# Kernel tuning notes

Hardware: AMD Instinct MI355X
Metric: run time of the kernel (lower is better)

## Reference

```python
import jax, jax.numpy as jnp
import numpy as np

D = 768        # d_model
NH = 12        # num_heads
HD = D // NH   # head_dim = 64
MH = 3072      # mlp_hidden = 4*d_model
EPS = 1e-5
SCALE = HD ** -0.5


def _ln(x, w, b):
    m = jnp.mean(x, axis=-1, keepdims=True)
    v = jnp.mean(jnp.square(x - m), axis=-1, keepdims=True)
    return (x - m) * jax.lax.rsqrt(v + EPS) * w + b


def _rotate_half(x):
    x1, x2 = jnp.split(x, 2, axis=-1)
    return jnp.concatenate([-x2, x1], axis=-1)


def _rope_cos_sin(n, dim):
    inv = 1.0 / (10000.0 ** (jnp.arange(0, dim, 2, dtype=jnp.float32) / dim))
    ang = jnp.arange(n, dtype=jnp.float32)[:, None] * inv[None, :]
    ang = jnp.concatenate([ang, ang], axis=-1)  # (n, dim)
    return jnp.cos(ang), jnp.sin(ang)


def _mlp(x, w1, b1, w2, b2):
    return jax.nn.gelu(x @ w1 + b1, approximate=False) @ w2 + b2


def _attn(q, k, v):
    # q,k,v: (B, S, NH, HD)
    a = jnp.einsum('bqhd,bkhd->bhqk', q, k) * SCALE
    a = jax.nn.softmax(a, axis=-1)
    return jnp.einsum('bhqk,bkhd->bqhd', a, v)


def _spatial_attn(x, qkv_w, proj_w, proj_b):
    # x: (B, T, H, W, C); attention over H*W per frame with 2D RoPE
    B, T, H, W, C = x.shape
    BT, S = B * T, H * W
    qkv = x.reshape(BT, S, C) @ qkv_w
    q, k, v = jnp.split(qkv, 3, axis=-1)
    q = q.reshape(BT, S, NH, HD)
    k = k.reshape(BT, S, NH, HD)
    v = v.reshape(BT, S, NH, HD)
    half = HD // 2
    cos_h, sin_h = _rope_cos_sin(H, half)
    cos_w, sin_w = _rope_cos_sin(W, half)

    def rope2d(t):
        t = t.reshape(BT, H, W, NH, HD)
        t1, t2 = t[..., :half], t[..., half:]
        ch, sh = cos_h[None, :, None, None, :], sin_h[None, :, None, None, :]
        cw, sw = cos_w[None, None, :, None, :], sin_w[None, None, :, None, :]
        t1 = t1 * ch + _rotate_half(t1) * sh  # rotate by row position
        t2 = t2 * cw + _rotate_half(t2) * sw  # rotate by col position
        return jnp.concatenate([t1, t2], axis=-1).reshape(BT, S, NH, HD)

    out = _attn(rope2d(q), rope2d(k), v).reshape(BT, S, C) @ proj_w + proj_b
    return out.reshape(B, T, H, W, C)


def _temporal_attn(vp, vf, ap, af, qkv_w, proj_w, proj_b):
    # vp/vf: (B, T, S, C); ap/af: (B, T, C); joint attention over concatenated time axis
    B, T_p, S, C = vp.shape
    T_f = vf.shape[1]
    BS = B * S
    vps = vp.transpose(0, 2, 1, 3).reshape(BS, T_p, C)
    vfs = vf.transpose(0, 2, 1, 3).reshape(BS, T_f, C)
    aps = jnp.broadcast_to(ap[:, None], (B, S, T_p, C)).reshape(BS, T_p, C)
    afs = jnp.broadcast_to(af[:, None], (B, S, T_f, C)).reshape(BS, T_f, C)
    tok = jnp.concatenate([vps, vfs, aps, afs], axis=1)
    TT = tok.shape[1]
    qkv = tok @ qkv_w
    q, k, v = jnp.split(qkv, 3, axis=-1)
    q = q.reshape(BS, TT, NH, HD)
    k = k.reshape(BS, TT, NH, HD)
    v = v.reshape(BS, TT, NH, HD)
    cos, sin = _rope_cos_sin(TT, HD)
    rope1d = lambda t: t * cos[None, :, None, :] + _rotate_half(t) * sin[None, :, None, :]
    out = _attn(rope1d(q), rope1d(k), v).reshape(BS, TT, C) @ proj_w + proj_b
    vp_o = out[:, :T_p].reshape(B, S, T_p, C).transpose(0, 2, 1, 3)
    vf_o = out[:, T_p:T_p + T_f].reshape(B, S, T_f, C).transpose(0, 2, 1, 3)
    ap_o = out[:, T_p + T_f:T_p + T_f + T_p].reshape(B, S, T_p, C).mean(axis=1)
    af_o = out[:, T_p + T_f + T_p:].reshape(B, S, T_f, C).mean(axis=1)
    return vp_o, vf_o, ap_o, af_o


def _forward(v_p, v_f, a_p, a_f,
             sa_qkv_w, sa_proj_w, sa_proj_b,
             smlp_w1, smlp_b1, smlp_w2, smlp_b2,
             ta_qkv_w, ta_proj_w, ta_proj_b,
             ln1_w, ln1_b, ln2_w, ln2_b, ln3_w, ln3_b, ln4_w, ln4_b,
             fvp_w1, fvp_b1, fvp_w2, fvp_b2,
             fvf_w1, fvf_b1, fvf_w2, fvf_b2,
             fap_w1, fap_b1, fap_w2, fap_b2,
             faf_w1, faf_b1, faf_w2, faf_b2):
    # 1) shared spatial attention (video streams) + 2) shared video MLP, pre-norm residual
    def video_stage(x):
        x = x + _spatial_attn(_ln(x, ln1_w, ln1_b), sa_qkv_w, sa_proj_w, sa_proj_b)
        x = x + _mlp(_ln(x, ln2_w, ln2_b), smlp_w1, smlp_b1, smlp_w2, smlp_b2)
        return x
    v_p = video_stage(v_p)
    v_f = video_stage(v_f)
    B, T_p, H, W, C = v_p.shape
    T_f = v_f.shape[1]
    S = H * W
    vp_s = v_p.reshape(B, T_p, S, C)
    vf_s = v_f.reshape(B, T_f, S, C)
    # 3) joint temporal attention across all streams with 1D RoPE
    dvp, dvf, dap, daf = _temporal_attn(
        _ln(vp_s, ln3_w, ln3_b), _ln(vf_s, ln3_w, ln3_b),
        _ln(a_p, ln3_w, ln3_b), _ln(a_f, ln3_w, ln3_b),
        ta_qkv_w, ta_proj_w, ta_proj_b)
    vp_s = vp_s + dvp
    vf_s = vf_s + dvf
    a_p = a_p + dap
    a_f = a_f + daf
    # 4) distinct final MLP per stream
    vp_s = vp_s + _mlp(_ln(vp_s, ln4_w, ln4_b), fvp_w1, fvp_b1, fvp_w2, fvp_b2)
    vf_s = vf_s + _mlp(_ln(vf_s, ln4_w, ln4_b), fvf_w1, fvf_b1, fvf_w2, fvf_b2)
    a_p = a_p + _mlp(_ln(a_p, ln4_w, ln4_b), fap_w1, fap_b1, fap_w2, fap_b2)
    a_f = a_f + _mlp(_ln(a_f, ln4_w, ln4_b), faf_w1, faf_b1, faf_w2, faf_b2)
    return (vp_s.reshape(B, T_p, H, W, C), vf_s.reshape(B, T_f, H, W, C), a_p, a_f)


def setup_inputs() -> dict:
    B, T, H, W = 4, 8, 16, 16
    key = jax.random.key(0)
    kit = iter(jax.random.split(key, 48))
    def nrm(shape, s=0.02):
        return jax.random.normal(next(kit), shape, jnp.float32) * s
    inp = {
        'v_p': jax.random.normal(next(kit), (B, T, H, W, D), jnp.float32),
        'v_f': jax.random.normal(next(kit), (B, T, H, W, D), jnp.float32),
        'a_p': jax.random.normal(next(kit), (B, T, D), jnp.float32),
        'a_f': jax.random.normal(next(kit), (B, T, D), jnp.float32),
        'sa_qkv_w': nrm((D, 3 * D)),
        'sa_proj_w': nrm((D, D)),
        'sa_proj_b': jnp.zeros((D,), jnp.float32),
        'smlp_w1': nrm((D, MH)), 'smlp_b1': jnp.zeros((MH,), jnp.float32),
        'smlp_w2': nrm((MH, D)), 'smlp_b2': jnp.zeros((D,), jnp.float32),
        'ta_qkv_w': nrm((D, 3 * D)),
        'ta_proj_w': nrm((D, D)),
        'ta_proj_b': jnp.zeros((D,), jnp.float32),
    }
    for nm in ('ln1', 'ln2', 'ln3', 'ln4'):
        inp[nm + '_w'] = jnp.ones((D,), jnp.float32)
        inp[nm + '_b'] = jnp.zeros((D,), jnp.float32)
    for nm in ('fvp', 'fvf', 'fap', 'faf'):
        inp[nm + '_w1'] = nrm((D, MH))
        inp[nm + '_b1'] = jnp.zeros((MH,), jnp.float32)
        inp[nm + '_w2'] = nrm((MH, D))
        inp[nm + '_b2'] = jnp.zeros((D,), jnp.float32)
    return inp


def reference(v_p, v_f, a_p, a_f,
              sa_qkv_w, sa_proj_w, sa_proj_b,
              smlp_w1, smlp_b1, smlp_w2, smlp_b2,
              ta_qkv_w, ta_proj_w, ta_proj_b,
              ln1_w, ln1_b, ln2_w, ln2_b, ln3_w, ln3_b, ln4_w, ln4_b,
              fvp_w1, fvp_b1, fvp_w2, fvp_b2,
              fvf_w1, fvf_b1, fvf_w2, fvf_b2,
              fap_w1, fap_b1, fap_w2, fap_b2,
              faf_w1, faf_b1, faf_w2, faf_b2):
    return _forward(v_p, v_f, a_p, a_f,
                    sa_qkv_w, sa_proj_w, sa_proj_b,
                    smlp_w1, smlp_b1, smlp_w2, smlp_b2,
                    ta_qkv_w, ta_proj_w, ta_proj_b,
                    ln1_w, ln1_b, ln2_w, ln2_b, ln3_w, ln3_b, ln4_w, ln4_b,
                    fvp_w1, fvp_b1, fvp_w2, fvp_b2,
                    fvf_w1, fvf_b1, fvf_w2, fvf_b2,
                    fap_w1, fap_b1, fap_w2, fap_b2,
                    faf_w1, faf_b1, faf_w2, faf_b2)
```

## Files before the change

kernel.cpp:

```cpp
#include <hip/hip_runtime.h>
#include <hip/hip_bf16.h>

#define D 768
#define NH 12
#define HD 64
#define MH 3072
#define LN_EPS 1e-5f
#define ATT_SCALE 0.125f

typedef unsigned short u16;
typedef unsigned int u32;
typedef short short8 __attribute__((ext_vector_type(8)));
typedef float f32x4 __attribute__((ext_vector_type(4)));

__device__ __forceinline__ float b2f(u16 u){
  union { u32 i; float f; } x; x.i = ((u32)u) << 16; return x.f;
}
__device__ __forceinline__ u16 f2b(float f){
  u32 x = __float_as_uint(f);
  x += 0x7fffu + ((x >> 16) & 1u);
  return (u16)(x >> 16);
}
__device__ __forceinline__ u32 packb(float a, float b){
  return (u32)f2b(a) | ((u32)f2b(b) << 16);
}
__device__ __forceinline__ bool is_f32(const u32* __restrict__ probe){
  return probe[0] == 0x3F800000u;
}

__device__ __forceinline__ void gload_lds16(const u16* g, u16* l){
  auto const* gp = reinterpret_cast<u32 const __attribute__((address_space(1)))*>(
      reinterpret_cast<uintptr_t>(g));
  auto* lp = reinterpret_cast<u32 __attribute__((address_space(3)))*>(
      reinterpret_cast<uintptr_t>(l));
  __builtin_amdgcn_global_load_lds(gp, lp, 16, 0, 0);
}

__device__ __forceinline__ void up8(uint4 u, float* f){
  f[0] = b2f((u16)(u.x & 0xffff)); f[1] = b2f((u16)(u.x >> 16));
  f[2] = b2f((u16)(u.y & 0xffff)); f[3] = b2f((u16)(u.y >> 16));
  f[4] = b2f((u16)(u.z & 0xffff)); f[5] = b2f((u16)(u.z >> 16));
  f[6] = b2f((u16)(u.w & 0xffff)); f[7] = b2f((u16)(u.w >> 16));
}

__global__ void k_in2f(const void* __restrict__ in, float* __restrict__ out, int n4,
                       const u32* __restrict__ probe){
  int i = blockIdx.x * 256 + threadIdx.x;
  if (i >= n4) return;
  if (is_f32(probe)){
    ((float4*)out)[i] = ((const float4*)in)[i];
  } else {
    uint2 u = ((const uint2*)in)[i];
    float4 f;
    f.x = b2f((u16)(u.x & 0xffff)); f.y = b2f((u16)(u.x >> 16));
    f.z = b2f((u16)(u.y & 0xffff)); f.w = b2f((u16)(u.y >> 16));
    ((float4*)out)[i] = f;
  }
}

__global__ void k_out(const float* __restrict__ in, void* __restrict__ out,
                      size_t elem_off, int n4, const u32* __restrict__ probe){
  int i = blockIdx.x * 256 + threadIdx.x;
  if (i >= n4) return;
  float4 f = ((const float4*)in)[i];
  if (is_f32(probe)){
    ((float4*)((float*)out + elem_off))[i] = f;
  } else {
    uint2 u;
    u.x = packb(f.x, f.y);
    u.y = packb(f.z, f.w);
    ((uint2*)((u16*)out + elem_off))[i] = u;
  }
}

__global__ __launch_bounds__(256) void k_transp(const void* __restrict__ W,
    u16* __restrict__ WT, int K, int N, const u32* __restrict__ probe)
{
  __shared__ u16 t[32][33];
  bool wf = is_f32(probe);
  int k0 = blockIdx.x * 32, n0 = blockIdx.y * 32;
  int tx = threadIdx.x & 31, ty = threadIdx.x >> 5;
  #pragma unroll
  for (int i = 0; i < 4; i++){
    int k = k0 + ty + i*8;
    float v = wf ? ((const float*)W)[(size_t)k*N + n0 + tx]
                 : b2f(((const u16*)W)[(size_t)k*N + n0 + tx]);
    t[ty + i*8][tx] = f2b(v);
  }
  __syncthreads();
  #pragma unroll
  for (int i = 0; i < 4; i++){
    int n = n0 + ty + i*8;
    WT[(size_t)n*K + k0 + tx] = t[tx][ty + i*8];
  }
}

__global__ __launch_bounds__(256) void k_ln(const float* __restrict__ X,
    const void* __restrict__ w, const void* __restrict__ b,
    u16* __restrict__ Y, int nrows, const u32* __restrict__ probe)
{
  bool wf = is_f32(probe);
  int wv = threadIdx.x >> 6, lane = threadIdx.x & 63;
  int row = blockIdx.x * 4 + wv;
  if (row >= nrows) return;
  const float* x = X + (size_t)row * D;
  float v[12];
  float s = 0.f;
  #pragma unroll
  for (int i = 0; i < 12; i++){ v[i] = x[lane + i*64]; s += v[i]; }
  #pragma unroll
  for (int m = 32; m; m >>= 1) s += __shfl_xor(s, m);
  float mean = s * (1.f/768.f);
  float q = 0.f;
  #pragma unroll
  for (int i = 0; i < 12; i++){ float d0 = v[i] - mean; q += d0*d0; }
  #pragma unroll
  for (int m = 32; m; m >>= 1) q += __shfl_xor(q, m);
  float rstd = rsqrtf(q * (1.f/768.f) + LN_EPS);
  u16* y = Y + (size_t)row * D;
  #pragma unroll
  for (int i = 0; i < 12; i++){
    int c = lane + i*64;
    float wc = wf ? ((const float*)w)[c] : b2f(((const u16*)w)[c]);
    float bc = wf ? ((const float*)b)[c] : b2f(((const u16*)b)[c]);
    y[c] = f2b((v[i] - mean) * rstd * wc + bc);
  }
}

#define BM 128
#define BK 64

template<int EPI, int GUARD, int BNN>
__global__ __launch_bounds__(256, 2) void k_gemm(
    const u16* __restrict__ A, const u16* __restrict__ WT,
    const void* __restrict__ bias, void* __restrict__ Cout,
    const float* __restrict__ resid, const u32* __restrict__ probe,
    int M, int N, int K)
{
  constexpr int AT = (BNN == 128) ? 4 : 2;
  __shared__ __align__(16) u16 lA[2][BM][BK];
  __shared__ __align__(16) u16 lB[2][BNN][BK];
  bool wf = is_f32(probe);
  int tid = threadIdx.x;
  int m0 = blockIdx.y * BM, n0 = blockIdx.x * BNN;
  int wv = tid >> 6, lane = tid & 63, quad = lane >> 4, r = lane & 15;
  int wm = (BNN == 128) ? (wv >> 1) * 64 : wv * 32;
  int wn = (BNN == 128) ? (wv & 1) * 64 : 0;

  f32x4 acc[AT][4] = {};

  int lrow = lane >> 3;
  int lcol = (lane & 7) * 8;
  int nt = K / BK;

  auto stage = [&](int t, int bi){
    int k0 = t * BK;
    if (GUARD){
      int a_r = tid >> 3;
      int a_c = (tid & 7) * 8;
      #pragma unroll
      for (int p = 0; p < 4; p++){
        int row = p*32 + a_r;
        uint4 val = make_uint4(0u,0u,0u,0u);
        if (m0 + row < M)
          val = *(const uint4*)(A + (size_t)(m0+row)*K + k0 + a_c);
        *(uint4*)&lA[bi][row][a_c] = val;
      }
    } else {
      #pragma unroll
      for (int p = 0; p < 4; p++){
        int c = wv*4 + p;
        gload_lds16(A + (size_t)(m0 + c*8 + lrow)*K + k0 + lcol, &lA[bi][c*8][0]);
      }
    }
    #pragma unroll
    for (int p = 0; p < BNN/32; p++){
      int c = wv*(BNN/32) + p;
      gload_lds16(WT + (size_t)(n0 + c*8 + lrow)*K + k0 + lcol, &lB[bi][c*8][0]);
    }
  };

  stage(0, 0);
  __syncthreads();

  for (int t = 0; t < nt; ++t){
    int cur = t & 1;
    if (t + 1 < nt) stage(t + 1, cur ^ 1);
    #pragma unroll
    for (int kk = 0; kk < 2; kk++){
      short8 af[AT], bf[4];
      #pragma unroll
      for (int i = 0; i < AT; i++)
        af[i] = *(const short8*)&lA[cur][wm + i*16 + r][kk*32 + quad*8];
      #pragma unroll
      for (int j = 0; j < 4; j++)
        bf[j] = *(const short8*)&lB[cur][wn + j*16 + r][kk*32 + quad*8];
      #pragma unroll
      for (int i = 0; i < AT; i++)
        #pragma unroll
        for (int j = 0; j < 4; j++)
          acc[i][j] = __builtin_amdgcn_mfma_f32_16x16x32_bf16(af[i], bf[j], acc[i][j], 0, 0, 0);
    }
    __syncthreads();
  }

  #pragma unroll
  for (int i = 0; i < AT; i++){
    #pragma unroll
    for (int reg = 0; reg < 4; reg++){
      int row = m0 + wm + i*16 + quad*4 + reg;
      if (row >= M) continue;
      #pragma unroll
      for (int j = 0; j < 4; j++){
        int col = n0 + wn + j*16 + r;
        float v = acc[i][j][reg];
        size_t idx = (size_t)row * N + col;
        if (EPI == 0){
          ((u16*)Cout)[idx] = f2b(v);
        } else if (EPI == 1){
          v += wf ? ((const float*)bias)[col] : b2f(((const u16*)bias)[col]);
          v = 0.5f * v * (1.f + erff(v * 0.70710678f));
          ((u16*)Cout)[idx] = f2b(v);
        } else {
          v += (wf ? ((const float*)bias)[col] : b2f(((const u16*)bias)[col])) + resid[idx];
          ((float*)Cout)[idx] = v;
        }
      }
    }
  }
}

__global__ __launch_bounds__(512, 2) void k_spat_attn(
    const u16* __restrict__ QKV, u16* __restrict__ OUT)
{
  __shared__ __align__(16) u16 lK[256*64];
  __shared__ __align__(16) u16 lVT[64*256];
  __shared__ __align__(16) u16 lQP[256*64];
  int bt = blockIdx.x / NH, h = blockIdx.x % NH;
  int tid = threadIdx.x;

  {
    int token = tid >> 1, half = tid & 1;
    int dbase = half * 32;
    float pos = half ? (float)(token & 15) : (float)(token >> 4);
    const u16* src = QKV + (size_t)(bt*256 + token) * 2304 + h*64 + dbase;
    float q[32], k[32];
    #pragma unroll
    for (int i = 0; i < 4; i++){
      up8(((const uint4*)src)[i],         &q[i*8]);
      up8(((const uint4*)(src + 768))[i], &k[i*8]);
    }
    #pragma unroll
    for (int j = 0; j < 16; j++){
      float inv = exp2f(-(float)j * 0.8304820237721841f);
      float sn, cs; __sincosf(pos * inv, &sn, &cs);
      { float a = q[j], b = q[j+16]; q[j] = a*cs - b*sn; q[j+16] = b*cs + a*sn; }
      { float a = k[j], b = k[j+16]; k[j] = a*cs - b*sn; k[j+16] = b*cs + a*sn; }
    }
    #pragma unroll
    for (int g = 0; g < 4; g++){
      int slot = (half*4 + g) ^ (token & 7);
      u32 wq[4], wk[4];
      #pragma unroll
      for (int p2 = 0; p2 < 4; p2++){
        wq[p2] = packb(q[g*8+p2*2] * ATT_SCALE, q[g*8+p2*2+1] * ATT_SCALE);
        wk[p2] = packb(k[g*8+p2*2], k[g*8+p2*2+1]);
      }
      *(uint4*)&lQP[token*64 + slot*8] = *(uint4*)wq;
      *(uint4*)&lK [token*64 + slot*8] = *(uint4*)wk;
    }
    uint4 vv[4];
    #pragma unroll
    for (int i = 0; i < 4; i++) vv[i] = ((const uint4*)(src + 1536))[i];
    #pragma unroll
    for (int i = 0; i < 32; i++){
      int d = dbase + i;
      u32 w = ((const u32*)vv)[i >> 1];
      lVT[d*256 + (((token>>3) ^ (d&7))*8) + (token&7)] =
          (i & 1) ? (u16)(w >> 16) : (u16)(w & 0xffff);
    }
  }
  __syncthreads();

  int wv = tid >> 6, lane = tid & 63, quad = lane >> 4, r = lane & 15;

  short8 qa[2][2];
  #pragma unroll
  for (int qt = 0; qt < 2; qt++)
    #pragma unroll
    for (int dc = 0; dc < 2; dc++){
      int q = wv*32 + qt*16 + r;
      int slot = (dc*4 + quad) ^ (q & 7);
      qa[qt][dc] = *(const short8*)&lQP[q*64 + slot*8];
    }
  __syncthreads();

  u16* Pw = &lQP[wv * 1024];
  const short8 ones = {(short)0x3F80,(short)0x3F80,(short)0x3F80,(short)0x3F80,
                       (short)0x3F80,(short)0x3F80,(short)0x3F80,(short)0x3F80};
  f32x4 acc[2][4] = {};
  f32x4 lacc[2] = {};
  float mrow[2][4];
  #pragma unroll
  for (int qt = 0; qt < 2; qt++)
    #pragma unroll
    for (int rg = 0; rg < 4; rg++) mrow[qt][rg] = -1e30f;

  for (int c = 0; c < 8; c++){
    f32x4 s[2][2] = {};
    #pragma unroll
    for (int dc = 0; dc < 2; dc++){
      short8 bk[2];
      #pragma unroll
      for (int kt = 0; kt < 2; kt++){
        int kk = c*32 + kt*16 + r;
        int slot = (dc*4 + quad) ^ (kk & 7);
        bk[kt] = *(const short8*)&lK[kk*64 + slot*8];
      }
      #pragma unroll
      for (int qt = 0; qt < 2; qt++)
        #pragma unroll
        for (int kt = 0; kt < 2; kt++)
          s[qt][kt] = __builtin_amdgcn_mfma_f32_16x16x32_bf16(qa[qt][dc], bk[kt], s[qt][kt], 0, 0, 0);
    }
    #pragma unroll
    for (int qt = 0; qt < 2; qt++){
      float corr[4];
      #pragma unroll
      for (int rg = 0; rg < 4; rg++){
        float mx = fmaxf(s[qt][0][rg], s[qt][1][rg]);
        #pragma unroll
        for (int msk = 1; msk <= 8; msk <<= 1) mx = fmaxf(mx, __shfl_xor(mx, msk));
        float mn = fmaxf(mrow[qt][rg], mx);
        corr[rg] = __expf(mrow[qt][rg] - mn);
        mrow[qt][rg] = mn;
      }
      #pragma unroll
      for (int rg = 0; rg < 4; rg++) lacc[qt][rg] *= corr[rg];
      #pragma unroll
      for (int dt = 0; dt < 4; dt++)
        #pragma unroll
        for (int rg = 0; rg < 4; rg++) acc[qt][dt][rg] *= corr[rg];
      #pragma unroll
      for (int kt = 0; kt < 2; kt++)
        #pragma unroll
        for (int rg = 0; rg < 4; rg++){
          float p = __expf(s[qt][kt][rg] - mrow[qt][rg]);
          int qq = qt*16 + quad*4 + rg;
          int kk = kt*16 + r;
          Pw[qq*32 + (((kk>>3) ^ ((qq>>1)&3))*8) + (kk&7)] = f2b(p);
        }
    }
    short8 pa[2];
    #pragma unroll
    for (int qt = 0; qt < 2; qt++){
      int qq = qt*16 + r;
      int slot = quad ^ ((qq>>1)&3);
      pa[qt] = *(const short8*)&Pw[qq*32 + slot*8];
      lacc[qt] = __builtin_amdgcn_mfma_f32_16x16x32_bf16(pa[qt], ones, lacc[qt], 0, 0, 0);
    }
    #pragma unroll
    for (int dt = 0; dt < 4; dt++){
      int d = dt*16 + r;
      int slot = (c*4 + quad) ^ (d & 7);
      short8 bv = *(const short8*)&lVT[d*256 + slot*8];
      #pragma unroll
      for (int qt = 0; qt < 2; qt++)
        acc[qt][dt] = __builtin_amdgcn_mfma_f32_16x16x32_bf16(pa[qt], bv, acc[qt][dt], 0, 0, 0);
    }
  }

  #pragma unroll
  for (int qt = 0; qt < 2; qt++)
    #pragma unroll
    for (int rg = 0; rg < 4; rg++){
      float invl = 1.f / lacc[qt][rg];
      int row = bt*256 + wv*32 + qt*16 + quad*4 + rg;
      u16* dst = OUT + (size_t)row * 768 + h*64;
      #pragma unroll
      for (int dt = 0; dt < 4; dt++)
        dst[dt*16 + r] = f2b(acc[qt][dt][rg] * invl);
    }
}

__global__ __launch_bounds__(256, 2) void k_temp_attn(
    const u16* __restrict__ QKVv, const u16* __restrict__ QKVa,
    u16* __restrict__ OUTv, u16* __restrict__ SCR)
{
  __shared__ __align__(16) u16 lQP[4][32*64];
  __shared__ __align__(16) u16 lK [4][32*64];
  __shared__ __align__(16) u16 lVT[4][64*32];
  int bs = blockIdx.x; int b = bs >> 8, s = bs & 255;
  int tid = threadIdx.x;
  int wv = tid >> 6, lane = tid & 63, quad = lane >> 4, r = lane & 15;
  int t = lane >> 1, half = lane & 1;
  int dA = half*16, dB = half*16 + 32;

  const u16* rowp;
  if (t < 8)       rowp = QKVv + (size_t)((b*8 + t)*256 + s) * 2304;
  else if (t < 16) rowp = QKVv + (size_t)(8192 + (b*8 + t-8)*256 + s) * 2304;
  else if (t < 24) rowp = QKVa + (size_t)(b*8 + t-16) * 2304;
  else             rowp = QKVa + (size_t)(32 + b*8 + t-24) * 2304;

  float rsn[16], rcs[16];
  #pragma unroll
  for (int dd = 0; dd < 16; dd++){
    int j = dA + dd;
    float inv = exp2f(-(float)j * 0.4152410118860920f);
    __sincosf((float)t * inv, &rsn[dd], &rcs[dd]);
  }

  u16* Qw = lQP[wv]; u16* Kw = lK[wv]; u16* VTw = lVT[wv];

  #pragma unroll 1
  for (int hi = 0; hi < 3; hi++){
    int h = wv*3 + hi;
    const u16* src = rowp + h*64;

    {
      float qa_[32], ka_[32];
      up8(((const uint4*)(src + dA))[0],       &qa_[0]);
      up8(((const uint4*)(src + dA))[1],       &qa_[8]);
      up8(((const uint4*)(src + dB))[0],       &qa_[16]);
      up8(((const uint4*)(src + dB))[1],       &qa_[24]);
      up8(((const uint4*)(src + 768 + dA))[0], &ka_[0]);
      up8(((const uint4*)(src + 768 + dA))[1], &ka_[8]);
      up8(((const uint4*)(src + 768 + dB))[0], &ka_[16]);
      up8(((const uint4*)(src + 768 + dB))[1], &ka_[24]);
      #pragma unroll
      for (int dd = 0; dd < 16; dd++){
        float a = qa_[dd], p = qa_[16+dd];
        qa_[dd]    = a*rcs[dd] - p*rsn[dd];
        qa_[16+dd] = p*rcs[dd] + a*rsn[dd];
        float c = ka_[dd], d2 = ka_[16+dd];
        ka_[dd]    = c*rcs[dd] - d2*rsn[dd];
        ka_[16+dd] = d2*rcs[dd] + c*rsn[dd];
      }
      u32 wq[16], wk[16];
      #pragma unroll
      for (int p = 0; p < 16; p++){
        wq[p] = packb(qa_[2*p]*ATT_SCALE, qa_[2*p+1]*ATT_SCALE);
        wk[p] = packb(ka_[2*p],           ka_[2*p+1]);
      }
      #pragma unroll
      for (int g = 0; g < 4; g++){
        int sl = ((g & 1) + ((g >> 1) << 2) + half*2) ^ (t & 7);
        *(uint4*)&Qw[t*64 + sl*8] = *(uint4*)&wq[g*4];
        *(uint4*)&Kw[t*64 + sl*8] = *(uint4*)&wk[g*4];
      }
    }
    {
      u32 vw[16];
      *(uint4*)&vw[0]  = ((const uint4*)(src + 1536 + dA))[0];
      *(uint4*)&vw[4]  = ((const uint4*)(src + 1536 + dA))[1];
      *(uint4*)&vw[8]  = ((const uint4*)(src + 1536 + dB))[0];
      *(uint4*)&vw[12] = ((const uint4*)(src + 1536 + dB))[1];
      #pragma unroll
      for (int i = 0; i < 32; i++){
        int d = (i < 16) ? (dA + i) : (dB + i - 16);
        u16 val = (i & 1) ? (u16)(vw[i>>1] >> 16) : (u16)(vw[i>>1] & 0xffff);
        VTw[d*32 + (((t>>3) ^ (d&3))*8) + (t&7)] = val;
      }
    }

    short8 qa[2][2];
    #pragma unroll
    for (int qt = 0; qt < 2; qt++)
      #pragma unroll
      for (int dc = 0; dc < 2; dc++){
        int q = qt*16 + r;
        int slot = (dc*4 + quad) ^ (q & 7);
        qa[qt][dc] = *(const short8*)&Qw[q*64 + slot*8];
      }
    f32x4 sv[2][2] = {};
    #pragma unroll
    for (int dc = 0; dc < 2; dc++){
      short8 bk[2];
      #pragma unroll
      for (int kt = 0; kt < 2; kt++){
        int kk = kt*16 + r;
        int slot = (dc*4 + quad) ^ (kk & 7);
        bk[kt] = *(const short8*)&Kw[kk*64 + slot*8];
      }
      #pragma unroll
      for (int qt = 0; qt < 2; qt++)
        #pragma unroll
        for (int kt = 0; kt < 2; kt++)
          sv[qt][kt] = __builtin_amdgcn_mfma_f32_16x16x32_bf16(qa[qt][dc], bk[kt], sv[qt][kt], 0, 0, 0);
    }

    u16* Pw = Qw;
    float linv[2][4];
    #pragma unroll
    for (int qt = 0; qt < 2; qt++){
      #pragma unroll
      for (int rg = 0; rg < 4; rg++){
        float mx = fmaxf(sv[qt][0][rg], sv[qt][1][rg]);
        #pragma unroll
        for (int msk = 1; msk <= 8; msk <<= 1) mx = fmaxf(mx, __shfl_xor(mx, msk));
        int qq = qt*16 + quad*4 + rg;
        float sum = 0.f;
        #pragma unroll
        for (int kt = 0; kt < 2; kt++){
          float p = __expf(sv[qt][kt][rg] - mx);
          u16 pq = f2b(p);
          sum += b2f(pq);
          int kk = kt*16 + r;
          Pw[qq*32 + (((kk>>3) ^ ((qq>>1)&3))*8) + (kk&7)] = pq;
        }
        #pragma unroll
        for (int msk = 1; msk <= 8; msk <<= 1) sum += __shfl_xor(sum, msk);
        linv[qt][rg] = 1.f / sum;
      }
    }

    short8 pa[2];
    #pragma unroll
    for (int qt = 0; qt < 2; qt++){
      int qq = qt*16 + r;
      int slot = quad ^ ((qq>>1)&3);
      pa[qt] = *(const short8*)&Pw[qq*32 + slot*8];
    }
    f32x4 oacc[2][4] = {};
    #pragma unroll
    for (int dt = 0; dt < 4; dt++){
      int d = dt*16 + r;
      int slot = quad ^ (d & 3);
      short8 bv = *(const short8*)&VTw[d*32 + slot*8];
      #pragma unroll
      for (int qt = 0; qt < 2; qt++)
        oacc[qt][dt] = __builtin_amdgcn_mfma_f32_16x16x32_bf16(pa[qt], bv, oacc[qt][dt], 0, 0, 0);
    }

    #pragma unroll
    for (int rg = 0; rg < 4; rg++){
      int token = quad*4 + rg;
      size_t orow = (token < 8) ? (size_t)((b*8 + token)*256 + s)
                                : (size_t)(8192 + (b*8 + token-8)*256 + s);
      u16* dst = OUTv + orow*768 + h*64;
      #pragma unroll
      for (int dt = 0; dt < 4; dt++)
        dst[dt*16 + r] = f2b(oacc[0][dt][rg] * linv[0][rg]);
    }
    #pragma unroll
    for (int rg = 0; rg < 4; rg++){
      int token = quad*4 + rg;
      u16* dst = SCR + ((size_t)bs*16 + token)*768 + h*64;
      #pragma unroll
      for (int dt = 0; dt < 4; dt++)
        dst[dt*16 + r] = f2b(oacc[1][dt][rg] * linv[1][rg]);
    }
  }
}

__global__ void k_audio_reduce(const u16* __restrict__ SCR, u16* __restrict__ OUT){
  int r = blockIdx.x;
  int b, tok;
  if (r < 32){ b = r >> 3; tok = r & 7; }
  else       { int rr = r - 32; b = rr >> 3; tok = 8 + (rr & 7); }
  for (int d = threadIdx.x; d < 768; d += 256){
    float acc = 0.f;
    for (int s2 = 0; s2 < 256; s2++)
      acc += b2f(SCR[((size_t)(b*256 + s2)*16 + tok)*768 + d]);
    OUT[(size_t)r*768 + d] = f2b(acc * (1.f/256.f));
  }
}

extern "C" void kernel_launch(void* const* d_in, const int* in_sizes, int n_in,
                              void* d_out, int out_size, void* d_ws, size_t ws_size,
                              hipStream_t stream)
{
  (void)in_sizes; (void)n_in; (void)out_size; (void)ws_size;
  const void* v_p_i    = d_in[0];
  const void* v_f_i    = d_in[1];
  const void* a_p_i    = d_in[2];
  const void* a_f_i    = d_in[3];
  const void* sa_qkv_w = d_in[4];
  const void* sa_proj_w= d_in[5];
  const void* sa_proj_b= d_in[6];
  const void* smlp_w1  = d_in[7];
  const void* smlp_b1  = d_in[8];
  const void* smlp_w2  = d_in[9];
  const void* smlp_b2  = d_in[10];
  const void* ta_qkv_w = d_in[11];
  const void* ta_proj_w= d_in[12];
  const void* ta_proj_b= d_in[13];
  const void* ln1_w = d_in[14];
  const void* ln1_b = d_in[15];
  const void* ln2_w = d_in[16];
  const void* ln2_b = d_in[17];
  const void* ln3_w = d_in[18];
  const void* ln3_b = d_in[19];
  const void* ln4_w = d_in[20];
  const void* ln4_b = d_in[21];
  const void* fvp_w1= d_in[22];
  const void* fvp_b1= d_in[23];
  const void* fvp_w2= d_in[24];
  const void* fvp_b2= d_in[25];
  const void* fvf_w1= d_in[26];
  const void* fvf_b1= d_in[27];
  const void* fvf_w2= d_in[28];
  const void* fvf_b2= d_in[29];
  const void* fap_w1= d_in[30];
  const void* fap_b1= d_in[31];
  const void* fap_w2= d_in[32];
  const void* fap_b2= d_in[33];
  const void* faf_w1= d_in[34];
  const void* faf_b1= d_in[35];
  const void* faf_w2= d_in[36];
  const void* faf_b2= d_in[37];
  const u32* probe = (const u32*)ln1_w;

  char* ws = (char*)d_ws;
  float* XP  = (float*)(ws + 0);
  float* XF  = (float*)(ws + 25165824);
  float* AP  = (float*)(ws + 50331648);
  float* AF  = (float*)(ws + 50429952);
  u16*  LN   = (u16*)(ws + 50528256);
  u16*  SCR  = LN;
  u16*  QKV  = (u16*)(ws + 75694080);
  u16*  HB   = QKV;
  u16*  ATTN = (u16*)(ws + 151191552);
  u16*  ALN  = (u16*)(ws + 176357376);
  u16*  AQKV = (u16*)(ws + 176455680);
  u16*  AATT = (u16*)(ws + 176750592);
  u16*  AH   = (u16*)(ws + 176848896);
  u16*  WT_SAQKV = (u16*)(ws + 177242112);
  u16*  WT_SAPRJ = (u16*)(ws + 180781056);
  u16*  WT_SMLP1 = (u16*)(ws + 181960704);
  u16*  WT_SMLP2 = (u16*)(ws + 186679296);
  u16*  WTS      = (u16*)(ws + 191397888);

  auto transp = [&](const void* Wm, u16* WT, int K, int N){
    dim3 g(K/32, N/32);
    k_transp<<<g, 256, 0, stream>>>(Wm, WT, K, N, probe);
  };

  auto gemm = [&](int EPI_, const u16* Ap, const u16* WTp, const void* bias,
                  void* Cp, const float* resid, int M, int N, int K){
    bool g = (M % 128) != 0;
    bool n64 = ((size_t)(N/128)) * ((M+127)/128) < 512;
    dim3 grid(N / (n64 ? 64 : 128), (M+127)/128);
    #define LG(E,G,B) k_gemm<E,G,B><<<grid,256,0,stream>>>(Ap,WTp,bias,Cp,resid,probe,M,N,K)
    if (EPI_ == 0){
      if (g){ if (n64) LG(0,1,64); else LG(0,1,128); }
      else  { if (n64) LG(0,0,64); else LG(0,0,128); }
    } else if (EPI_ == 1){
      if (g){ if (n64) LG(1,1,64); else LG(1,1,128); }
      else  { if (n64) LG(1,0,64); else LG(1,0,128); }
    } else {
      if (g){ if (n64) LG(2,1,64); else LG(2,1,128); }
      else  { if (n64) LG(2,0,64); else LG(2,0,128); }
    }
    #undef LG
  };
  auto gemm0 = [&](const u16* A, const u16* WT, u16* C, int M, int N, int K){
    gemm(0, A, WT, (const void*)nullptr, (void*)C, (const float*)nullptr, M, N, K);
  };
  auto gemm1 = [&](const u16* A, const u16* WT, const void* bias, u16* C, int M, int N, int K){
    gemm(1, A, WT, bias, (void*)C, (const float*)nullptr, M, N, K);
  };
  auto gemm2 = [&](const u16* A, const u16* WT, const void* bias, float* C, int M, int N, int K){
    gemm(2, A, WT, bias, (void*)C, (const float*)C, M, N, K);
  };

  transp(sa_qkv_w,  WT_SAQKV, 768, 2304);
  transp(sa_proj_w, WT_SAPRJ, 768, 768);
  transp(smlp_w1,   WT_SMLP1, 768, 3072);
  transp(smlp_w2,   WT_SMLP2, 3072, 768);

  const void* vids[2] = {v_p_i, v_f_i};
  float* Xs[2] = {XP, XF};
  for (int v = 0; v < 2; v++){
    k_in2f<<<6144, 256, 0, stream>>>(vids[v], Xs[v], 6291456/4, probe);
    k_ln<<<2048, 256, 0, stream>>>(Xs[v], ln1_w, ln1_b, LN, 8192, probe);
    gemm0(LN, WT_SAQKV, QKV, 8192, 2304, 768);
    k_spat_attn<<<384, 512, 0, stream>>>(QKV, ATTN);
    gemm2(ATTN, WT_SAPRJ, sa_proj_b, Xs[v], 8192, 768, 768);
    k_ln<<<2048, 256, 0, stream>>>(Xs[v], ln2_w, ln2_b, LN, 8192, probe);
    gemm1(LN, WT_SMLP1, smlp_b1, HB, 8192, 3072, 768);
    gemm2(HB, WT_SMLP2, smlp_b2, Xs[v], 8192, 768, 3072);
  }

  k_in2f<<<24, 256, 0, stream>>>(a_p_i, AP, 24576/4, probe);
  k_in2f<<<24, 256, 0, stream>>>(a_f_i, AF, 24576/4, probe);
  k_ln<<<4096, 256, 0, stream>>>(XP, ln3_w, ln3_b, LN, 16384, probe);
  k_ln<<<16, 256, 0, stream>>>(AP, ln3_w, ln3_b, ALN, 64, probe);
  transp(ta_qkv_w, WTS, 768, 2304);
  gemm0(LN, WTS, QKV, 16384, 2304, 768);
  gemm0(ALN, WTS, AQKV, 64, 2304, 768);
  k_temp_attn<<<1024, 256, 0, stream>>>(QKV, AQKV, ATTN, SCR);
  k_audio_reduce<<<64, 256, 0, stream>>>(SCR, AATT);
  transp(ta_proj_w, WTS, 768, 768);
  gemm2(ATTN, WTS, ta_proj_b, XP, 16384, 768, 768);
  gemm2(AATT, WTS, ta_proj_b, AP, 64, 768, 768);

  k_ln<<<4096, 256, 0, stream>>>(XP, ln4_w, ln4_b, LN, 16384, probe);
  k_ln<<<16, 256, 0, stream>>>(AP, ln4_w, ln4_b, ALN, 64, probe);
  transp(fvp_w1, WTS, 768, 3072);
  gemm1(LN, WTS, fvp_b1, HB, 8192, 3072, 768);
  transp(fvp_w2, WTS, 3072, 768);
  gemm2(HB, WTS, fvp_b2, XP, 8192, 768, 3072);
  transp(fvf_w1, WTS, 768, 3072);
  gemm1(LN + (size_t)8192*768, WTS, fvf_b1, HB, 8192, 3072, 768);
  transp(fvf_w2, WTS, 3072, 768);
  gemm2(HB, WTS, fvf_b2, XF, 8192, 768, 3072);
  transp(fap_w1, WTS, 768, 3072);
  gemm1(ALN, WTS, fap_b1, AH, 32, 3072, 768);
  transp(fap_w2, WTS, 3072, 768);
  gemm2(AH, WTS, fap_b2, AP, 32, 768, 3072);
  transp(faf_w1, WTS, 768, 3072);
  gemm1(ALN + (size_t)32*768, WTS, faf_b1, AH, 32, 3072, 768);
  transp(faf_w2, WTS, 3072, 768);
  gemm2(AH, WTS, faf_b2, AF, 32, 768, 3072);

  k_out<<<12288, 256, 0, stream>>>(XP, d_out, 0,        12582912/4, probe);
  k_out<<<48,    256, 0, stream>>>(AP, d_out, 12582912, 49152/4,    probe);
}
```

Baseline: 1.743 ms.

## Swizzle GEMM LDS tiles and batch both video streams into single passes

The GEMM's shared-memory tiles for A and B now use an XOR swizzle. The 16-byte chunk column is XORed with the row index on both the staging path and the MFMA fragment reads, so fragment loads no longer hit the same LDS banks. Separately, the per-stream loop over the past and future video is replaced by single launches over M=16384. This relies on XP and XF sitting next to each other in the workspace. The batched pass halves the launch count and gives larger grids for the LN, QKV, attention and MLP kernels, but the bigger MLP hidden buffer now reaches into the ATTN region, which is only safe because ATTN is dead by then.

```diff
diff --git a/kernel.cpp b/kernel.cpp
--- a/kernel.cpp
+++ b/kernel.cpp
@@ -150,33 +150,33 @@
   f32x4 acc[AT][4] = {};
 
   int lrow = lane >> 3;
-  int lcol = (lane & 7) * 8;
+  int scol = ((lane & 7) ^ lrow) * 8;
   int nt = K / BK;
 
   auto stage = [&](int t, int bi){
     int k0 = t * BK;
     if (GUARD){
       int a_r = tid >> 3;
-      int a_c = (tid & 7) * 8;
+      int a_sl = tid & 7;
       #pragma unroll
       for (int p = 0; p < 4; p++){
         int row = p*32 + a_r;
         uint4 val = make_uint4(0u,0u,0u,0u);
         if (m0 + row < M)
-          val = *(const uint4*)(A + (size_t)(m0+row)*K + k0 + a_c);
-        *(uint4*)&lA[bi][row][a_c] = val;
+          val = *(const uint4*)(A + (size_t)(m0+row)*K + k0 + a_sl*8);
+        *(uint4*)&lA[bi][row][(a_sl ^ (row & 7)) * 8] = val;
       }
     } else {
       #pragma unroll
       for (int p = 0; p < 4; p++){
         int c = wv*4 + p;
-        gload_lds16(A + (size_t)(m0 + c*8 + lrow)*K + k0 + lcol, &lA[bi][c*8][0]);
+        gload_lds16(A + (size_t)(m0 + c*8 + lrow)*K + k0 + scol, &lA[bi][c*8][0]);
       }
     }
     #pragma unroll
     for (int p = 0; p < BNN/32; p++){
       int c = wv*(BNN/32) + p;
-      gload_lds16(WT + (size_t)(n0 + c*8 + lrow)*K + k0 + lcol, &lB[bi][c*8][0]);
+      gload_lds16(WT + (size_t)(n0 + c*8 + lrow)*K + k0 + scol, &lB[bi][c*8][0]);
     }
   };
 
@@ -191,10 +191,10 @@
       short8 af[AT], bf[4];
       #pragma unroll
       for (int i = 0; i < AT; i++)
-        af[i] = *(const short8*)&lA[cur][wm + i*16 + r][kk*32 + quad*8];
+        af[i] = *(const short8*)&lA[cur][wm + i*16 + r][((kk*4 + quad) ^ (r & 7)) * 8];
       #pragma unroll
       for (int j = 0; j < 4; j++)
-        bf[j] = *(const short8*)&lB[cur][wn + j*16 + r][kk*32 + quad*8];
+        bf[j] = *(const short8*)&lB[cur][wn + j*16 + r][((kk*4 + quad) ^ (r & 7)) * 8];
       #pragma unroll
       for (int i = 0; i < AT; i++)
         #pragma unroll
@@ -620,6 +620,7 @@
   u16*  SCR  = LN;
   u16*  QKV  = (u16*)(ws + 75694080);
   u16*  HB   = QKV;
+  u16*  HB16 = QKV;
   u16*  ATTN = (u16*)(ws + 151191552);
   u16*  ALN  = (u16*)(ws + 176357376);
   u16*  AQKV = (u16*)(ws + 176455680);
@@ -669,18 +670,15 @@
   transp(smlp_w1,   WT_SMLP1, 768, 3072);
   transp(smlp_w2,   WT_SMLP2, 3072, 768);
 
-  const void* vids[2] = {v_p_i, v_f_i};
-  float* Xs[2] = {XP, XF};
-  for (int v = 0; v < 2; v++){
-    k_in2f<<<6144, 256, 0, stream>>>(vids[v], Xs[v], 6291456/4, probe);
-    k_ln<<<2048, 256, 0, stream>>>(Xs[v], ln1_w, ln1_b, LN, 8192, probe);
-    gemm0(LN, WT_SAQKV, QKV, 8192, 2304, 768);
-    k_spat_attn<<<384, 512, 0, stream>>>(QKV, ATTN);
-    gemm2(ATTN, WT_SAPRJ, sa_proj_b, Xs[v], 8192, 768, 768);
-    k_ln<<<2048, 256, 0, stream>>>(Xs[v], ln2_w, ln2_b, LN, 8192, probe);
-    gemm1(LN, WT_SMLP1, smlp_b1, HB, 8192, 3072, 768);
-    gemm2(HB, WT_SMLP2, smlp_b2, Xs[v], 8192, 768, 3072);
-  }
+  k_in2f<<<6144, 256, 0, stream>>>(v_p_i, XP, 6291456/4, probe);
+  k_in2f<<<6144, 256, 0, stream>>>(v_f_i, XF, 6291456/4, probe);
+  k_ln<<<4096, 256, 0, stream>>>(XP, ln1_w, ln1_b, LN, 16384, probe);
+  gemm0(LN, WT_SAQKV, QKV, 16384, 2304, 768);
+  k_spat_attn<<<768, 512, 0, stream>>>(QKV, ATTN);
+  gemm2(ATTN, WT_SAPRJ, sa_proj_b, XP, 16384, 768, 768);
+  k_ln<<<4096, 256, 0, stream>>>(XP, ln2_w, ln2_b, LN, 16384, probe);
+  gemm1(LN, WT_SMLP1, smlp_b1, HB16, 16384, 3072, 768);
+  gemm2(HB16, WT_SMLP2, smlp_b2, XP, 16384, 768, 3072);
 
   k_in2f<<<24, 256, 0, stream>>>(a_p_i, AP, 24576/4, probe);
   k_in2f<<<24, 256, 0, stream>>>(a_f_i, AF, 24576/4, probe);
```

Result: faster. 1.641 ms (-5.9%).
